# Kernel tuning notes

Hardware: AMD Instinct MI355X
Metric: run time of the kernel (lower is better)

## Reference

```python
import jax, jax.numpy as jnp
import numpy as np

B = 4096          # batch
L = 4096          # lattice_size (64x64)
N = L // 2        # n_masked
H = 2048          # hidden_size


def setup_inputs() -> dict:
    key = jax.random.key(0)
    ks = jax.random.split(key, 4)
    scale = 0.02  # small init so exp(s) stays tame (s is already bounded by 2*tanh)
    x = jax.random.normal(ks[0], (B, L), dtype=jnp.float32)
    W1 = jax.random.normal(ks[1], (N, H), dtype=jnp.float32) * scale
    b1 = jnp.zeros((H,), jnp.float32)
    W2 = jax.random.normal(ks[2], (H, H), dtype=jnp.float32) * scale
    b2 = jnp.zeros((H,), jnp.float32)
    W3 = jax.random.normal(ks[3], (H, 2 * N), dtype=jnp.float32) * scale
    b3 = jnp.zeros((2 * N,), jnp.float32)
    # checkerboard mask: even sites frozen (masked), odd sites transformed
    idx_masked = jnp.arange(0, L, 2, dtype=jnp.int32)
    idx_unmasked = jnp.arange(1, L, 2, dtype=jnp.int32)
    return {"x": x, "W1": W1, "b1": b1, "W2": W2, "b2": b2,
            "W3": W3, "b3": b3,
            "idx_masked": idx_masked, "idx_unmasked": idx_unmasked}


def reference(x, W1, b1, W2, b2, W3, b3, idx_masked, idx_unmasked):
    # gather frozen half: (B, N)
    x_m = x[:, idx_masked]
    # 3-layer MLP with LeakyReLU(0.2)
    h = jax.nn.leaky_relu(x_m @ W1 + b1, negative_slope=0.2)
    h = jax.nn.leaky_relu(h @ W2 + b2, negative_slope=0.2)
    out = h @ W3 + b3                      # (B, 2N)
    s, t = out[:, :N], out[:, N:]
    s = 2.0 * jnp.tanh(s)
    # affine transform of the unmasked half, scatter back
    x_u = x[:, idx_unmasked]
    y_u = x_u * jnp.exp(s) + t
    y = x.at[:, idx_unmasked].set(y_u)
    log_det = s.sum(axis=1)                # (B,)
    return y, log_det
```

## Files before the change

### kernel.cpp

```cpp
#include <hip/hip_runtime.h>
#include <hip/hip_bf16.h>
#include <stdint.h>

#define MROWS 4096
#define LFULL 4096
#define NHALF 2048
#define HDIM  2048

typedef __bf16 bf16x8 __attribute__((ext_vector_type(8)));
typedef float  f32x4  __attribute__((ext_vector_type(4)));
typedef unsigned short u16x8 __attribute__((ext_vector_type(8)));

template<int V> struct ICt { static constexpr int value = V; };

__device__ __forceinline__ unsigned short f2bf(float f) {
    __hip_bfloat16 h = __float2bfloat16(f);
    return __builtin_bit_cast(unsigned short, h);
}
__device__ __forceinline__ float bf2f(unsigned short u) {
    return __builtin_bit_cast(float, (uint32_t)u << 16);
}
__device__ __forceinline__ float fast_tanh(float x) {
    float ax = fabsf(x);
    float e  = __expf(-2.0f * ax);
    float t  = (1.0f - e) / (1.0f + e);
    return copysignf(t, x);
}

__device__ __forceinline__ void gload_lds16(const void* g, void* l) {
    __builtin_amdgcn_global_load_lds(
        (const __attribute__((address_space(1))) uint32_t*)g,
        (__attribute__((address_space(3))) uint32_t*)l,
        16, 0, 0);
}

__device__ __forceinline__ void transpose_body(
    const float* __restrict__ W, __hip_bfloat16* __restrict__ WT,
    int K, int N, int bx, int by, bool perm,
    unsigned short (*lds)[66], int t)
{
    const int k0 = by * 64;
    const int n0 = bx * 64;

    #pragma unroll
    for (int it = 0; it < 4; ++it) {
        int kl = it * 16 + (t >> 4);
        int nl = (t & 15) * 4;
        float4 v = *(const float4*)(W + (size_t)(k0 + kl) * N + n0 + nl);
        lds[kl][nl + 0] = f2bf(v.x);
        lds[kl][nl + 1] = f2bf(v.y);
        lds[kl][nl + 2] = f2bf(v.z);
        lds[kl][nl + 3] = f2bf(v.w);
    }
    __syncthreads();

    int nl = t >> 2;
    int kc = (t & 3) * 16;
    unsigned short tmp[16];
    #pragma unroll
    for (int j = 0; j < 16; ++j) tmp[j] = lds[kc + j][nl];
    int jc = n0 + nl;
    int dstrow;
    if (perm) {
        int half = jc >> 11;
        int j    = jc & 2047;
        dstrow = (j >> 7) * 256 + ((j >> 5) & 3) * 64
               + ((j & 1) + 2 * half) * 16 + ((j & 31) >> 1);
    } else {
        dstrow = jc;
    }
    u16x8* dst = (u16x8*)(WT + (size_t)dstrow * K + k0 + kc);
    dst[0] = *(u16x8*)&tmp[0];
    dst[1] = *(u16x8*)&tmp[8];
}

__global__ __launch_bounds__(256)
void prep_kernel(const float* __restrict__ x, __hip_bfloat16* __restrict__ xm,
                 float* __restrict__ ld,
                 const float* __restrict__ W1, __hip_bfloat16* __restrict__ W1T,
                 const float* __restrict__ W2, __hip_bfloat16* __restrict__ W2T,
                 const float* __restrict__ W3, __hip_bfloat16* __restrict__ W3T)
{
    __shared__ unsigned short lds[64][66];
    const int bid = blockIdx.x;
    const int t   = threadIdx.x;

    if (bid < 4096) {
        if (t == 0) ld[bid] = 0.0f;
        const size_t r = bid;
        const float4* xp = (const float4*)(x + r * LFULL + (size_t)t * 16);
        float4 a = xp[0], b = xp[1], d = xp[2], e = xp[3];
        u16x8 v;
        v[0] = f2bf(a.x); v[1] = f2bf(a.z);
        v[2] = f2bf(b.x); v[3] = f2bf(b.z);
        v[4] = f2bf(d.x); v[5] = f2bf(d.z);
        v[6] = f2bf(e.x); v[7] = f2bf(e.z);
        *(u16x8*)(xm + r * NHALF + (size_t)t * 8) = v;
    } else if (bid < 5120) {
        int b = bid - 4096;
        transpose_body(W1, W1T, HDIM, HDIM, b & 31, b >> 5, false, lds, t);
    } else if (bid < 6144) {
        int b = bid - 5120;
        transpose_body(W2, W2T, HDIM, HDIM, b & 31, b >> 5, false, lds, t);
    } else {
        int b = bid - 6144;
        transpose_body(W3, W3T, HDIM, LFULL, b & 63, b >> 6, true, lds, t);
    }
}

template<int BM, int BN, int KD, int NOUT, bool RELU, bool FUSED>
__global__ __launch_bounds__(512)
void gemm8p(const __hip_bfloat16* __restrict__ A,
            const __hip_bfloat16* __restrict__ BT,
            const float* __restrict__ bias,
            __hip_bfloat16* __restrict__ C,
            const float* __restrict__ xg,
            float* __restrict__ yg,
            float* __restrict__ ldg)
{
    constexpr int MF = BM / 32, NF = BN / 64, MH = MF / 2, NH = NF / 2;
    constexpr int LA = BM / 128, LB = BN / 128;
    constexpr int NT = KD / 64;
    constexpr int ABYTES = BM * 128, BBYTES = BN * 128;
    constexpr int BBASE = 2 * ABYTES;
    __shared__ __align__(1024) char lds[2 * ABYTES + 2 * BBYTES];

    const int tid  = threadIdx.x;
    const int wave = tid >> 6, lane = tid & 63;
    const int wm = wave >> 2, wn = wave & 3;
    const int l15 = lane & 15, lhi = lane >> 4;

    const int nwg = gridDim.x;
    const int bid = blockIdx.x;
    const int wg  = (bid & 7) * (nwg >> 3) + (bid >> 3);
    constexpr int NBN = NOUT / BN;
    const int bm = wg / NBN, bn = wg % NBN;

    const __hip_bfloat16* gA = A  + (size_t)(bm * BM) * KD;
    const __hip_bfloat16* gB = BT + (size_t)(bn * BN) * KD;

    const int srow = tid >> 3;
    const int scol = ((tid & 7) ^ (srow & 7)) * 8;
    char* sd = lds + srow * 128 + (tid & 7) * 16;

    const __hip_bfloat16* pA = gA + (size_t)srow * KD + scol;
    const __hip_bfloat16* pB = gB + (size_t)srow * KD + scol;

    #pragma unroll
    for (int s = 0; s < LB; ++s) gload_lds16(pB + (size_t)(s * 64) * KD,             sd + BBASE + s * 8192);
    #pragma unroll
    for (int s = 0; s < LB; ++s) gload_lds16(pB + (size_t)(BN/2 + s * 64) * KD,      sd + BBASE + (BN/2) * 128 + s * 8192);
    #pragma unroll
    for (int s = 0; s < LA; ++s) gload_lds16(pA + (size_t)(s * 64) * KD,             sd + s * 8192);
    #pragma unroll
    for (int s = 0; s < LA; ++s) gload_lds16(pA + (size_t)(BM/2 + s * 64) * KD,      sd + (BM/2) * 128 + s * 8192);
    #pragma unroll
    for (int s = 0; s < LB; ++s) gload_lds16(pB + 64 + (size_t)(s * 64) * KD,        sd + BBASE + BBYTES + s * 8192);
    #pragma unroll
    for (int s = 0; s < LB; ++s) gload_lds16(pB + 64 + (size_t)(BN/2 + s * 64) * KD, sd + BBASE + BBYTES + (BN/2) * 128 + s * 8192);
    pA += 64; pB += 128;
    asm volatile("s_waitcnt vmcnt(4)" ::: "memory");
    __builtin_amdgcn_s_barrier();

    const int arow0 = wm * (BM / 2) + l15;
    const int brow0 = wn * (BN / 4) + l15;
    const int swz   = (l15 & 7) << 4;
    const int colX[2] = { (lhi * 16) ^ swz, (64 + lhi * 16) ^ swz };
    const char* rA = lds + arow0 * 128;
    const char* rB = lds + brow0 * 128;

    bf16x8 af[MH][2], bf0[NH][2], bf1[NH][2];
    f32x4 acc[MF][NF] = {};

    #pragma unroll
    for (int m = 0; m < MH; ++m)
        #pragma unroll
        for (int kk = 0; kk < 2; ++kk)
            af[m][kk] = *(const bf16x8*)(rA + colX[kk] + m * 2048);
    #pragma unroll
    for (int n = 0; n < NH; ++n)
        #pragma unroll
        for (int kk = 0; kk < 2; ++kk)
            bf0[n][kk] = *(const bf16x8*)(rB + colX[kk] + (BBASE + n * 2048));

    auto body = [&](int t, auto bufc) {
        constexpr int BUF   = decltype(bufc)::value;
        constexpr int ABUF  = BUF * ABYTES;
        constexpr int ABUFo = (BUF ^ 1) * ABYTES;
        constexpr int BBUF  = BBASE + BUF * BBYTES;
        constexpr int BBUFo = BBASE + (BUF ^ 1) * BBYTES;

        if (t + 1 < NT) {
            #pragma unroll
            for (int s = 0; s < LA; ++s)
                gload_lds16(pA + (size_t)(s * 64) * KD, sd + ABUFo + s * 8192);
        }
        __builtin_amdgcn_s_setprio(1);
        #pragma unroll
        for (int kk = 0; kk < 2; ++kk)
            #pragma unroll
            for (int m = 0; m < MH; ++m)
                #pragma unroll
                for (int n = 0; n < NH; ++n)
                    acc[m][n] = __builtin_amdgcn_mfma_f32_16x16x32_bf16(af[m][kk], bf0[n][kk], acc[m][n], 0, 0, 0);
        __builtin_amdgcn_s_setprio(0);
        #pragma unroll
        for (int n = 0; n < NH; ++n)
            #pragma unroll
            for (int kk = 0; kk < 2; ++kk)
                bf1[n][kk] = *(const bf16x8*)(rB + colX[kk] + (BBUF + (NH + n) * 2048));

        if (t + 1 < NT) {
            #pragma unroll
            for (int s = 0; s < LA; ++s)
                gload_lds16(pA + (size_t)(BM/2 + s * 64) * KD, sd + ABUFo + (BM/2) * 128 + s * 8192);
        }
        __builtin_amdgcn_s_setprio(1);
        #pragma unroll
        for (int kk = 0; kk < 2; ++kk)
            #pragma unroll
            for (int m = 0; m < MH; ++m)
                #pragma unroll
                for (int n = 0; n < NH; ++n)
                    acc[m][NH + n] = __builtin_amdgcn_mfma_f32_16x16x32_bf16(af[m][kk], bf1[n][kk], acc[m][NH + n], 0, 0, 0);
        __builtin_amdgcn_s_setprio(0);
        #pragma unroll
        for (int m = 0; m < MH; ++m)
            #pragma unroll
            for (int kk = 0; kk < 2; ++kk)
                af[m][kk] = *(const bf16x8*)(rA + colX[kk] + (ABUF + (MH + m) * 2048));
        __builtin_amdgcn_s_barrier();

        if (t + 2 < NT) {
            #pragma unroll
            for (int s = 0; s < LB; ++s)
                gload_lds16(pB + (size_t)(s * 64) * KD, sd + BBUF + s * 8192);
        }
        __builtin_amdgcn_s_setprio(1);
        #pragma unroll
        for (int kk = 0; kk < 2; ++kk)
            #pragma unroll
            for (int m = 0; m < MH; ++m)
                #pragma unroll
                for (int n = 0; n < NH; ++n)
                    acc[MH + m][n] = __builtin_amdgcn_mfma_f32_16x16x32_bf16(af[m][kk], bf0[n][kk], acc[MH + m][n], 0, 0, 0);
        __builtin_amdgcn_s_setprio(0);

        if (t + 2 < NT) {
            #pragma unroll
            for (int s = 0; s < LB; ++s)
                gload_lds16(pB + (size_t)(BN/2 + s * 64) * KD, sd + BBUF + (BN/2) * 128 + s * 8192);
            asm volatile("s_waitcnt vmcnt(4)" ::: "memory");
        } else {
            asm volatile("s_waitcnt vmcnt(0)" ::: "memory");
        }
        __builtin_amdgcn_s_barrier();
        if (t + 1 < NT) {
            #pragma unroll
            for (int n = 0; n < NH; ++n)
                #pragma unroll
                for (int kk = 0; kk < 2; ++kk)
                    bf0[n][kk] = *(const bf16x8*)(rB + colX[kk] + (BBUFo + n * 2048));
        }
        __builtin_amdgcn_s_setprio(1);
        #pragma unroll
        for (int kk = 0; kk < 2; ++kk)
            #pragma unroll
            for (int m = 0; m < MH; ++m)
                #pragma unroll
                for (int n = 0; n < NH; ++n)
                    acc[MH + m][NH + n] = __builtin_amdgcn_mfma_f32_16x16x32_bf16(af[m][kk], bf1[n][kk], acc[MH + m][NH + n], 0, 0, 0);
        __builtin_amdgcn_s_setprio(0);
        if (t + 1 < NT) {
            #pragma unroll
            for (int m = 0; m < MH; ++m)
                #pragma unroll
                for (int kk = 0; kk < 2; ++kk)
                    af[m][kk] = *(const bf16x8*)(rA + colX[kk] + (ABUFo + m * 2048));
        }
        pA += 64; pB += 64;
    };

    for (int tt = 0; tt < NT; tt += 2) {
        body(tt,     ICt<0>{});
        body(tt + 1, ICt<1>{});
    }

    const int crow0 = bm * BM + wm * (BM / 2) + lhi * 4;
    if constexpr (FUSED) {
        const int j0 = bn * (BN / 2) + wn * 32 + 2 * l15;
        const float2 sbv = *(const float2*)(bias + j0);
        const float2 tbv = *(const float2*)(bias + NHALF + j0);
        #pragma unroll
        for (int m = 0; m < MF; ++m) {
            #pragma unroll
            for (int r = 0; r < 4; ++r) {
                const int row = crow0 + m * 16 + r;
                float s0 = acc[m][0][r] + sbv.x;
                float s1 = acc[m][1][r] + sbv.y;
                float t0 = acc[m][2][r] + tbv.x;
                float t1 = acc[m][3][r] + tbv.y;
                float a0 = 2.0f * fast_tanh(s0);
                float a1 = 2.0f * fast_tanh(s1);
                float4 xv = *(const float4*)(xg + (size_t)row * LFULL + 2 * j0);
                float4 yv;
                yv.x = xv.x;
                yv.y = xv.y * __expf(a0) + t0;
                yv.z = xv.z;
                yv.w = xv.w * __expf(a1) + t1;
                *(float4*)(yg + (size_t)row * LFULL + 2 * j0) = yv;
                float ldp = a0 + a1;
                ldp += __shfl_xor(ldp, 1, 64);
                ldp += __shfl_xor(ldp, 2, 64);
                ldp += __shfl_xor(ldp, 4, 64);
                ldp += __shfl_xor(ldp, 8, 64);
                if (l15 == 0) atomicAdd(&ldg[row], ldp);
            }
        }
    } else {
        const int ccol0 = bn * BN + wn * (BN / 4) + l15;
        #pragma unroll
        for (int m = 0; m < MF; ++m) {
            #pragma unroll
            for (int n = 0; n < NF; ++n) {
                int col = ccol0 + n * 16;
                float bv = bias[col];
                #pragma unroll
                for (int r = 0; r < 4; ++r) {
                    int row = crow0 + m * 16 + r;
                    float v = acc[m][n][r] + bv;
                    if (RELU) v = (v > 0.0f) ? v : 0.2f * v;
                    C[(size_t)row * NOUT + col] = __float2bfloat16(v);
                }
            }
        }
    }
}

extern "C" void kernel_launch(void* const* d_in, const int* in_sizes, int n_in,
                              void* d_out, int out_size, void* d_ws, size_t ws_size,
                              hipStream_t stream)
{
    const float* x  = (const float*)d_in[0];
    const float* W1 = (const float*)d_in[1];
    const float* b1 = (const float*)d_in[2];
    const float* W2 = (const float*)d_in[3];
    const float* b2 = (const float*)d_in[4];
    const float* W3 = (const float*)d_in[5];
    const float* b3 = (const float*)d_in[6];

    char* ws = (char*)d_ws;
    const size_t MB = 1u << 20;
    __hip_bfloat16* W3T  = (__hip_bfloat16*)(ws);
    __hip_bfloat16* h2   = (__hip_bfloat16*)(ws + 16 * MB);
    __hip_bfloat16* xmb  = (__hip_bfloat16*)(ws + 32 * MB);
    __hip_bfloat16* W1T  = (__hip_bfloat16*)(ws + 48 * MB);
    __hip_bfloat16* W2T  = (__hip_bfloat16*)(ws + 56 * MB);
    __hip_bfloat16* h1   = (__hip_bfloat16*)(ws + 64 * MB);

    float* y  = (float*)d_out;
    float* ld = y + (size_t)MROWS * LFULL;

    prep_kernel<<<8192, 256, 0, stream>>>(x, xmb, ld, W1, W1T, W2, W2T, W3, W3T);

    gemm8p<128, 256, 2048, 2048, true,  false><<<dim3(256), dim3(512), 0, stream>>>(xmb, W1T, b1, h1, nullptr, nullptr, nullptr);
    gemm8p<128, 256, 2048, 2048, true,  false><<<dim3(256), dim3(512), 0, stream>>>(h1,  W2T, b2, h2, nullptr, nullptr, nullptr);
    gemm8p<256, 256, 2048, 4096, false, true ><<<dim3(256), dim3(512), 0, stream>>>(h2,  W3T, b3, nullptr, x, y, ld);
}
```

Before: 176.6 us.

## Use 32x32x16 MFMA GEMM kernel for first two MLP layers

Adds a new GEMM kernel built on the 32x32x16 bf16 MFMA instruction instead of the 16x16 variant, with a 2x2 per-wave fragment layout, double-buffered LDS and staged global-to-LDS loads. It is used for the first two hidden layers, while the fused last layer keeps the old kernel. The larger MFMA tile is meant to cut LDS fragment reads per flop and raise matrix-core throughput. The epilogue writes bf16 scalars with a strided pattern, which may cost store efficiency.

```diff
diff --git a/kernel.cpp b/kernel.cpp
--- a/kernel.cpp
+++ b/kernel.cpp
@@ -9,6 +9,7 @@
 
 typedef __bf16 bf16x8 __attribute__((ext_vector_type(8)));
 typedef float  f32x4  __attribute__((ext_vector_type(4)));
+typedef float  f32x16 __attribute__((ext_vector_type(16)));
 typedef unsigned short u16x8 __attribute__((ext_vector_type(8)));
 
 template<int V> struct ICt { static constexpr int value = V; };
@@ -105,6 +106,171 @@
     } else {
         int b = bid - 6144;
         transpose_body(W3, W3T, HDIM, LFULL, b & 63, b >> 6, true, lds, t);
+    }
+}
+
+template<int BM, int BN, int KD, int NOUT, bool RELU>
+__global__ __launch_bounds__(512)
+void gemm32(const __hip_bfloat16* __restrict__ A,
+            const __hip_bfloat16* __restrict__ BT,
+            const float* __restrict__ bias,
+            __hip_bfloat16* __restrict__ C)
+{
+    constexpr int LA = BM / 128, LB = BN / 128;
+    constexpr int NT = KD / 64;
+    constexpr int ABYTES = BM * 128, BBYTES = BN * 128;
+    constexpr int BBASE = 2 * ABYTES;
+    __shared__ __align__(1024) char lds[2 * ABYTES + 2 * BBYTES];
+
+    const int tid  = threadIdx.x;
+    const int wave = tid >> 6, lane = tid & 63;
+    const int wm = wave >> 2, wn = wave & 3;
+    const int l31 = lane & 31, khalf = lane >> 5;
+
+    const int nwg = gridDim.x;
+    const int bid = blockIdx.x;
+    const int wg  = (bid & 7) * (nwg >> 3) + (bid >> 3);
+    constexpr int NBN = NOUT / BN;
+    const int bm = wg / NBN, bn = wg % NBN;
+
+    const __hip_bfloat16* gA = A  + (size_t)(bm * BM) * KD;
+    const __hip_bfloat16* gB = BT + (size_t)(bn * BN) * KD;
+
+    const int srow = tid >> 3;
+    const int scol = ((tid & 7) ^ (srow & 7)) * 8;
+    char* sd = lds + srow * 128 + (tid & 7) * 16;
+
+    const __hip_bfloat16* pA = gA + (size_t)srow * KD + scol;
+    const __hip_bfloat16* pB = gB + (size_t)srow * KD + scol;
+
+    #pragma unroll
+    for (int s = 0; s < LB; ++s) gload_lds16(pB + (size_t)(s * 64) * KD,             sd + BBASE + s * 8192);
+    #pragma unroll
+    for (int s = 0; s < LB; ++s) gload_lds16(pB + (size_t)(BN/2 + s * 64) * KD,      sd + BBASE + (BN/2) * 128 + s * 8192);
+    #pragma unroll
+    for (int s = 0; s < LA; ++s) gload_lds16(pA + (size_t)(s * 64) * KD,             sd + s * 8192);
+    #pragma unroll
+    for (int s = 0; s < LA; ++s) gload_lds16(pA + (size_t)(BM/2 + s * 64) * KD,      sd + (BM/2) * 128 + s * 8192);
+    #pragma unroll
+    for (int s = 0; s < LB; ++s) gload_lds16(pB + 64 + (size_t)(s * 64) * KD,        sd + BBASE + BBYTES + s * 8192);
+    #pragma unroll
+    for (int s = 0; s < LB; ++s) gload_lds16(pB + 64 + (size_t)(BN/2 + s * 64) * KD, sd + BBASE + BBYTES + (BN/2) * 128 + s * 8192);
+    pA += 64; pB += 128;
+    asm volatile("s_waitcnt vmcnt(4)" ::: "memory");
+    __builtin_amdgcn_s_barrier();
+
+    const int arow0 = wm * 64 + l31;
+    const int brow0 = wn * 64 + l31;
+    const int swz   = (lane & 7) << 4;
+    int colK[4];
+    #pragma unroll
+    for (int ks = 0; ks < 4; ++ks) colK[ks] = (ks * 32 + khalf * 16) ^ swz;
+    const char* rA = lds + arow0 * 128;
+    const char* rB = lds + brow0 * 128;
+
+    bf16x8 af[4], bf0[4], bf1[4];
+    f32x16 acc[2][2] = {};
+
+    #pragma unroll
+    for (int ks = 0; ks < 4; ++ks) af[ks]  = *(const bf16x8*)(rA + colK[ks]);
+    #pragma unroll
+    for (int ks = 0; ks < 4; ++ks) bf0[ks] = *(const bf16x8*)(rB + colK[ks] + BBASE);
+
+    auto body = [&](int t, auto bufc) {
+        constexpr int BUF   = decltype(bufc)::value;
+        constexpr int ABUF  = BUF * ABYTES;
+        constexpr int ABUFo = (BUF ^ 1) * ABYTES;
+        constexpr int BBUF  = BBASE + BUF * BBYTES;
+        constexpr int BBUFo = BBASE + (BUF ^ 1) * BBYTES;
+
+        if (t + 1 < NT) {
+            #pragma unroll
+            for (int s = 0; s < LA; ++s)
+                gload_lds16(pA + (size_t)(s * 64) * KD, sd + ABUFo + s * 8192);
+        }
+        __builtin_amdgcn_s_setprio(1);
+        #pragma unroll
+        for (int ks = 0; ks < 4; ++ks)
+            acc[0][0] = __builtin_amdgcn_mfma_f32_32x32x16_bf16(af[ks], bf0[ks], acc[0][0], 0, 0, 0);
+        __builtin_amdgcn_s_setprio(0);
+        #pragma unroll
+        for (int ks = 0; ks < 4; ++ks)
+            bf1[ks] = *(const bf16x8*)(rB + colK[ks] + (BBUF + 4096));
+
+        if (t + 1 < NT) {
+            #pragma unroll
+            for (int s = 0; s < LA; ++s)
+                gload_lds16(pA + (size_t)(BM/2 + s * 64) * KD, sd + ABUFo + (BM/2) * 128 + s * 8192);
+        }
+        __builtin_amdgcn_s_setprio(1);
+        #pragma unroll
+        for (int ks = 0; ks < 4; ++ks)
+            acc[0][1] = __builtin_amdgcn_mfma_f32_32x32x16_bf16(af[ks], bf1[ks], acc[0][1], 0, 0, 0);
+        __builtin_amdgcn_s_setprio(0);
+        #pragma unroll
+        for (int ks = 0; ks < 4; ++ks)
+            af[ks] = *(const bf16x8*)(rA + colK[ks] + (ABUF + 4096));
+        __builtin_amdgcn_s_barrier();
+
+        if (t + 2 < NT) {
+            #pragma unroll
+            for (int s = 0; s < LB; ++s)
+                gload_lds16(pB + (size_t)(s * 64) * KD, sd + BBUF + s * 8192);
+        }
+        __builtin_amdgcn_s_setprio(1);
+        #pragma unroll
+        for (int ks = 0; ks < 4; ++ks)
+            acc[1][0] = __builtin_amdgcn_mfma_f32_32x32x16_bf16(af[ks], bf0[ks], acc[1][0], 0, 0, 0);
+        __builtin_amdgcn_s_setprio(0);
+
+        if (t + 2 < NT) {
+            #pragma unroll
+            for (int s = 0; s < LB; ++s)
+                gload_lds16(pB + (size_t)(BN/2 + s * 64) * KD, sd + BBUF + (BN/2) * 128 + s * 8192);
+            asm volatile("s_waitcnt vmcnt(4)" ::: "memory");
+        } else {
+            asm volatile("s_waitcnt vmcnt(0)" ::: "memory");
+        }
+        __builtin_amdgcn_s_barrier();
+        if (t + 1 < NT) {
+            #pragma unroll
+            for (int ks = 0; ks < 4; ++ks)
+                bf0[ks] = *(const bf16x8*)(rB + colK[ks] + BBUFo);
+        }
+        __builtin_amdgcn_s_setprio(1);
+        #pragma unroll
+        for (int ks = 0; ks < 4; ++ks)
+            acc[1][1] = __builtin_amdgcn_mfma_f32_32x32x16_bf16(af[ks], bf1[ks], acc[1][1], 0, 0, 0);
+        __builtin_amdgcn_s_setprio(0);
+        if (t + 1 < NT) {
+            #pragma unroll
+            for (int ks = 0; ks < 4; ++ks)
+                af[ks] = *(const bf16x8*)(rA + colK[ks] + ABUFo);
+        }
+        pA += 64; pB += 64;
+    };
+
+    for (int tt = 0; tt < NT; tt += 2) {
+        body(tt,     ICt<0>{});
+        body(tt + 1, ICt<1>{});
+    }
+
+    const int crow0 = bm * BM + wm * 64 + khalf * 4;
+    const int ccol0 = bn * BN + wn * 64 + l31;
+    #pragma unroll
+    for (int m = 0; m < 2; ++m) {
+        #pragma unroll
+        for (int n = 0; n < 2; ++n) {
+            int col = ccol0 + n * 32;
+            float bv = bias[col];
+            #pragma unroll
+            for (int reg = 0; reg < 16; ++reg) {
+                int row = crow0 + m * 32 + (reg & 3) + 8 * (reg >> 2);
+                float v = acc[m][n][reg] + bv;
+                if (RELU) v = (v > 0.0f) ? v : 0.2f * v;
+                C[(size_t)row * NOUT + col] = __float2bfloat16(v);
+            }
+        }
     }
 }
 
@@ -363,7 +529,7 @@
 
     prep_kernel<<<8192, 256, 0, stream>>>(x, xmb, ld, W1, W1T, W2, W2T, W3, W3T);
 
-    gemm8p<128, 256, 2048, 2048, true,  false><<<dim3(256), dim3(512), 0, stream>>>(xmb, W1T, b1, h1, nullptr, nullptr, nullptr);
-    gemm8p<128, 256, 2048, 2048, true,  false><<<dim3(256), dim3(512), 0, stream>>>(h1,  W2T, b2, h2, nullptr, nullptr, nullptr);
-    gemm8p<256, 256, 2048, 4096, false, true ><<<dim3(256), dim3(512), 0, stream>>>(h2,  W3T, b3, nullptr, x, y, ld);
-}
+    gemm32<128, 256, 2048, 2048, true><<<dim3(256), dim3(512), 0, stream>>>(xmb, W1T, b1, h1);
+    gemm32<128, 256, 2048, 2048, true><<<dim3(256), dim3(512), 0, stream>>>(h1,  W2T, b2, h2);
+    gemm8p<256, 256, 2048, 4096, false, true><<<dim3(256), dim3(512), 0, stream>>>(h2, W3T, b3, nullptr, x, y, ld);
+}
```

Measured after the change: 183.3 us. 3.8% more time.

## Switch GEMMs from 8 to 4 waves per block with larger per-wave tiles

Applied to the files above, without the earlier changes.

Rewrites the GEMM kernel to use 256 threads (4 waves in a 2x2 layout) instead of 512 (8 waves in 2x4), so each wave computes twice as many output columns. Global-to-LDS loads are split into more, smaller chunks, and the wait counts are parameterised to match. The W3 row permutation and the fused epilogue are updated for the new 64-column-per-wave mapping. The aim is more MFMA work per LDS fragment read and less barrier overhead per wave. In exchange, register pressure rises sharply and there are fewer waves to hide latency.

```diff
diff --git a/kernel.cpp b/kernel.cpp
--- a/kernel.cpp
+++ b/kernel.cpp
@@ -64,8 +64,7 @@
     if (perm) {
         int half = jc >> 11;
         int j    = jc & 2047;
-        dstrow = (j >> 7) * 256 + ((j >> 5) & 3) * 64
-               + ((j & 1) + 2 * half) * 16 + ((j & 31) >> 1);
+        dstrow = (j >> 5) * 64 + ((j & 1) + 2 * half) * 16 + ((j & 31) >> 1);
     } else {
         dstrow = jc;
     }
@@ -109,8 +108,8 @@
 }
 
 template<int BM, int BN, int KD, int NOUT, bool RELU, bool FUSED>
-__global__ __launch_bounds__(512)
-void gemm8p(const __hip_bfloat16* __restrict__ A,
+__global__ __launch_bounds__(256)
+void gemm4w(const __hip_bfloat16* __restrict__ A,
             const __hip_bfloat16* __restrict__ BT,
             const float* __restrict__ bias,
             __hip_bfloat16* __restrict__ C,
@@ -118,8 +117,9 @@
             float* __restrict__ yg,
             float* __restrict__ ldg)
 {
-    constexpr int MF = BM / 32, NF = BN / 64, MH = MF / 2, NH = NF / 2;
-    constexpr int LA = BM / 128, LB = BN / 128;
+    constexpr int MF = BM / 32, NF = BN / 32;
+    constexpr int MH = MF / 2, NH = NF / 2;
+    constexpr int LA = BM / 64, LB = BN / 64;
     constexpr int NT = KD / 64;
     constexpr int ABYTES = BM * 128, BBYTES = BN * 128;
     constexpr int BBASE = 2 * ABYTES;
@@ -127,7 +127,7 @@
 
     const int tid  = threadIdx.x;
     const int wave = tid >> 6, lane = tid & 63;
-    const int wm = wave >> 2, wn = wave & 3;
+    const int wm = wave >> 1, wn = wave & 1;
     const int l15 = lane & 15, lhi = lane >> 4;
 
     const int nwg = gridDim.x;
@@ -147,23 +147,23 @@
     const __hip_bfloat16* pB = gB + (size_t)srow * KD + scol;
 
     #pragma unroll
-    for (int s = 0; s < LB; ++s) gload_lds16(pB + (size_t)(s * 64) * KD,             sd + BBASE + s * 8192);
-    #pragma unroll
-    for (int s = 0; s < LB; ++s) gload_lds16(pB + (size_t)(BN/2 + s * 64) * KD,      sd + BBASE + (BN/2) * 128 + s * 8192);
-    #pragma unroll
-    for (int s = 0; s < LA; ++s) gload_lds16(pA + (size_t)(s * 64) * KD,             sd + s * 8192);
-    #pragma unroll
-    for (int s = 0; s < LA; ++s) gload_lds16(pA + (size_t)(BM/2 + s * 64) * KD,      sd + (BM/2) * 128 + s * 8192);
-    #pragma unroll
-    for (int s = 0; s < LB; ++s) gload_lds16(pB + 64 + (size_t)(s * 64) * KD,        sd + BBASE + BBYTES + s * 8192);
-    #pragma unroll
-    for (int s = 0; s < LB; ++s) gload_lds16(pB + 64 + (size_t)(BN/2 + s * 64) * KD, sd + BBASE + BBYTES + (BN/2) * 128 + s * 8192);
+    for (int s = 0; s < LB; ++s) gload_lds16(pB + (size_t)(s * 32) * KD,             sd + BBASE + s * 4096);
+    #pragma unroll
+    for (int s = 0; s < LB; ++s) gload_lds16(pB + (size_t)(BN/2 + s * 32) * KD,      sd + BBASE + (BN/2) * 128 + s * 4096);
+    #pragma unroll
+    for (int s = 0; s < LA; ++s) gload_lds16(pA + (size_t)(s * 32) * KD,             sd + s * 4096);
+    #pragma unroll
+    for (int s = 0; s < LA; ++s) gload_lds16(pA + (size_t)(BM/2 + s * 32) * KD,      sd + (BM/2) * 128 + s * 4096);
+    #pragma unroll
+    for (int s = 0; s < LB; ++s) gload_lds16(pB + 64 + (size_t)(s * 32) * KD,        sd + BBASE + BBYTES + s * 4096);
+    #pragma unroll
+    for (int s = 0; s < LB; ++s) gload_lds16(pB + 64 + (size_t)(BN/2 + s * 32) * KD, sd + BBASE + BBYTES + (BN/2) * 128 + s * 4096);
     pA += 64; pB += 128;
-    asm volatile("s_waitcnt vmcnt(4)" ::: "memory");
+    asm volatile("s_waitcnt vmcnt(%0)" :: "n"(2 * LB) : "memory");
     __builtin_amdgcn_s_barrier();
 
     const int arow0 = wm * (BM / 2) + l15;
-    const int brow0 = wn * (BN / 4) + l15;
+    const int brow0 = wn * (BN / 2) + l15;
     const int swz   = (l15 & 7) << 4;
     const int colX[2] = { (lhi * 16) ^ swz, (64 + lhi * 16) ^ swz };
     const char* rA = lds + arow0 * 128;
@@ -193,7 +193,7 @@
         if (t + 1 < NT) {
             #pragma unroll
             for (int s = 0; s < LA; ++s)
-                gload_lds16(pA + (size_t)(s * 64) * KD, sd + ABUFo + s * 8192);
+                gload_lds16(pA + (size_t)(s * 32) * KD, sd + ABUFo + s * 4096);
         }
         __builtin_amdgcn_s_setprio(1);
         #pragma unroll
@@ -213,7 +213,7 @@
         if (t + 1 < NT) {
             #pragma unroll
             for (int s = 0; s < LA; ++s)
-                gload_lds16(pA + (size_t)(BM/2 + s * 64) * KD, sd + ABUFo + (BM/2) * 128 + s * 8192);
+                gload_lds16(pA + (size_t)(BM/2 + s * 32) * KD, sd + ABUFo + (BM/2) * 128 + s * 4096);
         }
         __builtin_amdgcn_s_setprio(1);
         #pragma unroll
@@ -234,7 +234,7 @@
         if (t + 2 < NT) {
             #pragma unroll
             for (int s = 0; s < LB; ++s)
-                gload_lds16(pB + (size_t)(s * 64) * KD, sd + BBUF + s * 8192);
+                gload_lds16(pB + (size_t)(s * 32) * KD, sd + BBUF + s * 4096);
         }
         __builtin_amdgcn_s_setprio(1);
         #pragma unroll
@@ -249,8 +249,8 @@
         if (t + 2 < NT) {
             #pragma unroll
             for (int s = 0; s < LB; ++s)
-                gload_lds16(pB + (size_t)(BN/2 + s * 64) * KD, sd + BBUF + (BN/2) * 128 + s * 8192);
-            asm volatile("s_waitcnt vmcnt(4)" ::: "memory");
+                gload_lds16(pB + (size_t)(BN/2 + s * 32) * KD, sd + BBUF + (BN/2) * 128 + s * 4096);
+            asm volatile("s_waitcnt vmcnt(%0)" :: "n"(2 * LB) : "memory");
         } else {
             asm volatile("s_waitcnt vmcnt(0)" ::: "memory");
         }
@@ -288,28 +288,31 @@
 
     const int crow0 = bm * BM + wm * (BM / 2) + lhi * 4;
     if constexpr (FUSED) {
-        const int j0 = bn * (BN / 2) + wn * 32 + 2 * l15;
-        const float2 sbv = *(const float2*)(bias + j0);
-        const float2 tbv = *(const float2*)(bias + NHALF + j0);
+        const int jb = bn * (BN / 2) + wn * (BN / 4);
         #pragma unroll
         for (int m = 0; m < MF; ++m) {
             #pragma unroll
             for (int r = 0; r < 4; ++r) {
                 const int row = crow0 + m * 16 + r;
-                float s0 = acc[m][0][r] + sbv.x;
-                float s1 = acc[m][1][r] + sbv.y;
-                float t0 = acc[m][2][r] + tbv.x;
-                float t1 = acc[m][3][r] + tbv.y;
-                float a0 = 2.0f * fast_tanh(s0);
-                float a1 = 2.0f * fast_tanh(s1);
-                float4 xv = *(const float4*)(xg + (size_t)row * LFULL + 2 * j0);
-                float4 yv;
-                yv.x = xv.x;
-                yv.y = xv.y * __expf(a0) + t0;
-                yv.z = xv.z;
-                yv.w = xv.w * __expf(a1) + t1;
-                *(float4*)(yg + (size_t)row * LFULL + 2 * j0) = yv;
-                float ldp = a0 + a1;
+                float ldp = 0.0f;
+                #pragma unroll
+                for (int g = 0; g < 2; ++g) {
+                    const int j0 = jb + g * 32 + 2 * l15;
+                    float s0 = acc[m][4 * g + 0][r] + bias[j0];
+                    float s1 = acc[m][4 * g + 1][r] + bias[j0 + 1];
+                    float t0 = acc[m][4 * g + 2][r] + bias[NHALF + j0];
+                    float t1 = acc[m][4 * g + 3][r] + bias[NHALF + j0 + 1];
+                    float a0 = 2.0f * fast_tanh(s0);
+                    float a1 = 2.0f * fast_tanh(s1);
+                    float4 xv = *(const float4*)(xg + (size_t)row * LFULL + 2 * j0);
+                    float4 yv;
+                    yv.x = xv.x;
+                    yv.y = xv.y * __expf(a0) + t0;
+                    yv.z = xv.z;
+                    yv.w = xv.w * __expf(a1) + t1;
+                    *(float4*)(yg + (size_t)row * LFULL + 2 * j0) = yv;
+                    ldp += a0 + a1;
+                }
                 ldp += __shfl_xor(ldp, 1, 64);
                 ldp += __shfl_xor(ldp, 2, 64);
                 ldp += __shfl_xor(ldp, 4, 64);
@@ -318,7 +321,7 @@
             }
         }
     } else {
-        const int ccol0 = bn * BN + wn * (BN / 4) + l15;
+        const int ccol0 = bn * BN + wn * (BN / 2) + l15;
         #pragma unroll
         for (int m = 0; m < MF; ++m) {
             #pragma unroll
@@ -363,7 +366,7 @@
 
     prep_kernel<<<8192, 256, 0, stream>>>(x, xmb, ld, W1, W1T, W2, W2T, W3, W3T);
 
-    gemm8p<128, 256, 2048, 2048, true,  false><<<dim3(256), dim3(512), 0, stream>>>(xmb, W1T, b1, h1, nullptr, nullptr, nullptr);
-    gemm8p<128, 256, 2048, 2048, true,  false><<<dim3(256), dim3(512), 0, stream>>>(h1,  W2T, b2, h2, nullptr, nullptr, nullptr);
-    gemm8p<256, 256, 2048, 4096, false, true ><<<dim3(256), dim3(512), 0, stream>>>(h2,  W3T, b3, nullptr, x, y, ld);
-}
+    gemm4w<128, 256, 2048, 2048, true,  false><<<dim3(256), dim3(256), 0, stream>>>(xmb, W1T, b1, h1, nullptr, nullptr, nullptr);
+    gemm4w<128, 256, 2048, 2048, true,  false><<<dim3(256), dim3(256), 0, stream>>>(h1,  W2T, b2, h2, nullptr, nullptr, nullptr);
+    gemm4w<256, 256, 2048, 4096, false, true ><<<dim3(256), dim3(256), 0, stream>>>(h2,  W3T, b3, nullptr, x, y, ld);
+}
```

Result: slower. 389.9 us (+120.8%).
